# Kernel tuning notes

Hardware: AMD Instinct MI355X
Metric: run time of the kernel (lower is better)

## Reference

```python
import jax, jax.numpy as jnp
import numpy as np

N, E = 100000, 1600000
F_IN, F_HID, F_OUT = 512, 128, 16


def gcn_conv(x, W, b, src, dst, ew):
    """PyG GCNConv: h = x @ W; add self loops (weight 1); symmetric norm
    D^-1/2 A D^-1/2; aggregate messages to dst; add bias."""
    n = x.shape[0]
    loop = jnp.arange(n, dtype=src.dtype)
    s = jnp.concatenate([src, loop])
    d = jnp.concatenate([dst, loop])
    w = jnp.concatenate([ew, jnp.ones((n,), ew.dtype)])
    deg = jax.ops.segment_sum(w, d, num_segments=n)           # [N]
    dinv = jnp.where(deg > 0, jax.lax.rsqrt(deg), 0.0)
    norm = dinv[s] * w * dinv[d]                              # [E+N]
    h = x @ W                                                 # [N, out]
    out = jax.ops.segment_sum(h[s] * norm[:, None], d, num_segments=n)
    return out + b


def setup_inputs() -> dict:
    key = jax.random.key(0)
    k = jax.random.split(key, 5)
    x = jax.random.normal(k[0], (N, F_IN), jnp.float32)
    edge_index = jax.random.randint(k[1], (2, E), 0, N, jnp.int32)
    edge_weight = jnp.ones((E,), jnp.float32)
    W1 = jax.random.normal(k[2], (F_IN, F_HID), jnp.float32) * (1.0 / np.sqrt(F_IN))
    b1 = jnp.zeros((F_HID,), jnp.float32)
    W2 = jax.random.normal(k[3], (F_HID, F_OUT), jnp.float32) * (1.0 / np.sqrt(F_HID))
    b2 = jnp.zeros((F_OUT,), jnp.float32)
    return {"x": x, "edge_index": edge_index, "edge_weight": edge_weight,
            "W1": W1, "b1": b1, "W2": W2, "b2": b2}


def reference(x, edge_index, edge_weight, W1, b1, W2, b2):
    # eval mode: dropout is identity; use_ln=False, layer_norm_first=False
    src, dst = edge_index[0], edge_index[1]
    h = jax.nn.relu(gcn_conv(x, W1, b1, src, dst, edge_weight))
    logits = gcn_conv(h, W2, b2, src, dst, edge_weight)
    return jax.nn.log_softmax(logits, axis=1)
```

## Files before the change

kernel.cpp:

```cpp
#include <hip/hip_runtime.h>
#include <math.h>


#define F_IN 512
#define F_HID 128
#define F_OUT 16

__global__ __launch_bounds__(256) void k_cnt_deg(const int* __restrict__ dst,
                                                 const float* __restrict__ ew,
                                                 int* __restrict__ cnt,
                                                 float* __restrict__ degw, int E) {
  int e = blockIdx.x * 256 + threadIdx.x;
  if (e < E) {
    int d = dst[e];
    atomicAdd(&cnt[d], 1);
    atomicAdd(&degw[d], ew[e]);
  }
}

__global__ __launch_bounds__(256) void k_dinv(float* __restrict__ deg, int n) {
  int i = blockIdx.x * 256 + threadIdx.x;
  if (i < n) {
    float d = deg[i] + 1.0f;
    deg[i] = d > 0.f ? rsqrtf(d) : 0.f;
  }
}

__global__ __launch_bounds__(256) void k_scan1(const int* __restrict__ cnt,
                                               int* __restrict__ rowptr,
                                               int* __restrict__ bsum, int n) {
  __shared__ int sd[256];
  const int t = threadIdx.x;
  const int i = blockIdx.x * 256 + t;
  int v = (i < n) ? cnt[i] : 0;
  sd[t] = v;
  __syncthreads();
#pragma unroll
  for (int off = 1; off < 256; off <<= 1) {
    int add = (t >= off) ? sd[t - off] : 0;
    __syncthreads();
    sd[t] += add;
    __syncthreads();
  }
  if (i < n) rowptr[i] = sd[t] - v;
  if (t == 255) bsum[blockIdx.x] = sd[255];
}

__global__ __launch_bounds__(512) void k_scan2(int* __restrict__ bsum, int nb) {
  __shared__ int sd[512];
  const int t = threadIdx.x;
  int v = (t < nb) ? bsum[t] : 0;
  sd[t] = v;
  __syncthreads();
#pragma unroll
  for (int off = 1; off < 512; off <<= 1) {
    int add = (t >= off) ? sd[t - off] : 0;
    __syncthreads();
    sd[t] += add;
    __syncthreads();
  }
  if (t < nb) bsum[t] = sd[t] - v;
}

__global__ __launch_bounds__(256) void k_scan3(int* __restrict__ rowptr,
                                               const int* __restrict__ bsum,
                                               int* __restrict__ cursor,
                                               int n, int E) {
  int i = blockIdx.x * 256 + threadIdx.x;
  if (i < n) {
    int r = rowptr[i] + bsum[blockIdx.x];
    rowptr[i] = r;
    cursor[i] = r;
  }
  if (i == 0) rowptr[n] = E;
}

__global__ __launch_bounds__(256) void k_scatter(const int* __restrict__ src,
                                                 const int* __restrict__ dst,
                                                 const float* __restrict__ ew,
                                                 const float* __restrict__ dinv,
                                                 int* __restrict__ cursor,
                                                 int* __restrict__ es,
                                                 float* __restrict__ en, int E) {
  int e = blockIdx.x * 256 + threadIdx.x;
  if (e >= E) return;
  int s = src[e], d = dst[e];
  int pos = atomicAdd(&cursor[d], 1);
  es[pos] = s;
  en[pos] = dinv[s] * ew[e] * dinv[d];
}

__global__ __launch_bounds__(256) void k_gemm1(const float* __restrict__ A,
                                               const float* __restrict__ B,
                                               float* __restrict__ C, int n) {
  __shared__ float As[16][68];
  __shared__ float Bs[16][128];
  const int tid = threadIdx.x;
  const int bm = blockIdx.x * 64;
  const int ty = tid >> 4;
  const int tx = tid & 15;
  const int am = tid >> 2, ak = (tid & 3) << 2;
  const int bk = tid >> 4, bx = tid & 15;
  float acc[4][8];
#pragma unroll
  for (int i = 0; i < 4; ++i)
#pragma unroll
    for (int j = 0; j < 8; ++j) acc[i][j] = 0.f;

  for (int k0 = 0; k0 < F_IN; k0 += 16) {
    float4 av = make_float4(0.f, 0.f, 0.f, 0.f);
    if (bm + am < n)
      av = *reinterpret_cast<const float4*>(&A[(size_t)(bm + am) * F_IN + k0 + ak]);
    float4 b0 = *reinterpret_cast<const float4*>(&B[(size_t)(k0 + bk) * F_HID + bx * 4]);
    float4 b1 = *reinterpret_cast<const float4*>(&B[(size_t)(k0 + bk) * F_HID + 64 + bx * 4]);
    __syncthreads();
    As[ak + 0][am] = av.x;
    As[ak + 1][am] = av.y;
    As[ak + 2][am] = av.z;
    As[ak + 3][am] = av.w;
    *reinterpret_cast<float4*>(&Bs[bk][bx * 4]) = b0;
    *reinterpret_cast<float4*>(&Bs[bk][64 + bx * 4]) = b1;
    __syncthreads();
#pragma unroll
    for (int kk = 0; kk < 16; ++kk) {
      float4 a4 = *reinterpret_cast<const float4*>(&As[kk][ty * 4]);
      float4 p0 = *reinterpret_cast<const float4*>(&Bs[kk][tx * 4]);
      float4 p1 = *reinterpret_cast<const float4*>(&Bs[kk][64 + tx * 4]);
      float a[4] = {a4.x, a4.y, a4.z, a4.w};
      float b[8] = {p0.x, p0.y, p0.z, p0.w, p1.x, p1.y, p1.z, p1.w};
#pragma unroll
      for (int i = 0; i < 4; ++i)
#pragma unroll
        for (int j = 0; j < 8; ++j) acc[i][j] = fmaf(a[i], b[j], acc[i][j]);
    }
  }
#pragma unroll
  for (int i = 0; i < 4; ++i) {
    int r = bm + ty * 4 + i;
    if (r < n) {
      *reinterpret_cast<float4*>(&C[(size_t)r * F_HID + tx * 4]) =
          make_float4(acc[i][0], acc[i][1], acc[i][2], acc[i][3]);
      *reinterpret_cast<float4*>(&C[(size_t)r * F_HID + 64 + tx * 4]) =
          make_float4(acc[i][4], acc[i][5], acc[i][6], acc[i][7]);
    }
  }
}

__global__ __launch_bounds__(256) void k_pull128(const int* __restrict__ rowptr,
                                                 const int* __restrict__ es,
                                                 const float* __restrict__ en,
                                                 const float* __restrict__ h1,
                                                 const float* __restrict__ dinv,
                                                 const float* __restrict__ b1,
                                                 float* __restrict__ out, int n) {
  int node = blockIdx.x * 4 + (threadIdx.x >> 6);
  if (node >= n) return;
  int lane = threadIdx.x & 63;
  int beg = rowptr[node], end = rowptr[node + 1];
  float ax = 0.f, ay = 0.f;
  int j = beg;
  for (; j + 1 < end; j += 2) {
    int s0 = es[j], s1 = es[j + 1];
    float n0 = en[j], n1 = en[j + 1];
    float2 v0 = *reinterpret_cast<const float2*>(&h1[(size_t)s0 * F_HID + lane * 2]);
    float2 v1 = *reinterpret_cast<const float2*>(&h1[(size_t)s1 * F_HID + lane * 2]);
    ax = fmaf(v0.x, n0, ax);
    ay = fmaf(v0.y, n0, ay);
    ax = fmaf(v1.x, n1, ax);
    ay = fmaf(v1.y, n1, ay);
  }
  if (j < end) {
    int s0 = es[j];
    float n0 = en[j];
    float2 v0 = *reinterpret_cast<const float2*>(&h1[(size_t)s0 * F_HID + lane * 2]);
    ax = fmaf(v0.x, n0, ax);
    ay = fmaf(v0.y, n0, ay);
  }
  float di = dinv[node], sl = di * di;
  float2 hv = *reinterpret_cast<const float2*>(&h1[(size_t)node * F_HID + lane * 2]);
  float2 bv = *reinterpret_cast<const float2*>(&b1[lane * 2]);
  float2 r;
  r.x = fmaxf(fmaf(hv.x, sl, ax) + bv.x, 0.f);
  r.y = fmaxf(fmaf(hv.y, sl, ay) + bv.y, 0.f);
  *reinterpret_cast<float2*>(&out[(size_t)node * F_HID + lane * 2]) = r;
}

__global__ __launch_bounds__(256) void k_gemm2(const float* __restrict__ h,
                                               const float* __restrict__ W2,
                                               float* __restrict__ out, int n) {
  __shared__ float w2s[F_HID * F_OUT];
  for (int t = threadIdx.x; t < F_HID * F_OUT; t += 256) w2s[t] = W2[t];
  __syncthreads();
  int t = blockIdx.x * 256 + threadIdx.x;
  int i = t >> 4, j = t & 15;
  if (i >= n) return;
  const float4* row = reinterpret_cast<const float4*>(&h[(size_t)i * F_HID]);
  float acc = 0.f;
#pragma unroll
  for (int k4 = 0; k4 < F_HID / 4; ++k4) {
    float4 r = row[k4];
    acc = fmaf(r.x, w2s[(k4 * 4 + 0) * F_OUT + j], acc);
    acc = fmaf(r.y, w2s[(k4 * 4 + 1) * F_OUT + j], acc);
    acc = fmaf(r.z, w2s[(k4 * 4 + 2) * F_OUT + j], acc);
    acc = fmaf(r.w, w2s[(k4 * 4 + 3) * F_OUT + j], acc);
  }
  out[t] = acc;
}

__global__ __launch_bounds__(256) void k_pull16_out(const int* __restrict__ rowptr,
                                                    const int* __restrict__ es,
                                                    const float* __restrict__ en,
                                                    const float* __restrict__ h2,
                                                    const float* __restrict__ dinv,
                                                    const float* __restrict__ b2,
                                                    float* __restrict__ out, int n) {
  int node = blockIdx.x * 16 + (threadIdx.x >> 4);
  if (node >= n) return;
  int lane = threadIdx.x & 15;
  int beg = rowptr[node], end = rowptr[node + 1];
  float acc = 0.f;
  int j = beg;
  for (; j + 1 < end; j += 2) {
    float v0 = h2[(size_t)es[j] * F_OUT + lane];
    float v1 = h2[(size_t)es[j + 1] * F_OUT + lane];
    acc = fmaf(v0, en[j], acc);
    acc = fmaf(v1, en[j + 1], acc);
  }
  if (j < end) acc = fmaf(h2[(size_t)es[j] * F_OUT + lane], en[j], acc);
  float di = dinv[node];
  float v = fmaf(h2[(size_t)node * F_OUT + lane], di * di, acc) + b2[lane];
  float m = v;
#pragma unroll
  for (int off = 8; off; off >>= 1) m = fmaxf(m, __shfl_xor(m, off, 16));
  float ex = expf(v - m);
  float s = ex;
#pragma unroll
  for (int off = 8; off; off >>= 1) s += __shfl_xor(s, off, 16);
  out[(size_t)node * F_OUT + lane] = v - m - logf(s);
}

extern "C" void kernel_launch(void* const* d_in, const int* in_sizes, int n_in,
                              void* d_out, int out_size, void* d_ws, size_t ws_size,
                              hipStream_t stream) {
  const float* x  = (const float*)d_in[0];
  const int*   ei = (const int*)d_in[1];
  const float* ew = (const float*)d_in[2];
  const float* W1 = (const float*)d_in[3];
  const float* b1 = (const float*)d_in[4];
  const float* W2 = (const float*)d_in[5];
  const float* b2 = (const float*)d_in[6];
  float* out = (float*)d_out;

  const int fhid = in_sizes[4];
  const int fin  = in_sizes[3] / fhid;
  const int n = in_sizes[0] / fin;
  const int E = in_sizes[2];
  const int* src = ei;
  const int* dst = ei + E;

  const size_t nr = (size_t)((n + 255) & ~255);
  float* ws     = (float*)d_ws;
  float* dinv   = ws;
  float* h1     = dinv + nr;
  float* agg1   = h1 + (size_t)n * F_HID;
  float* h2     = agg1 + (size_t)n * F_HID;
  int*   cnt    = (int*)(h2 + (size_t)n * F_OUT);
  int*   rowptr = cnt + nr;
  int*   bsum   = rowptr + nr;
  int*   es     = bsum + 512;
  float* en     = (float*)(es + E);

  hipMemsetAsync(dinv, 0, nr * 4, stream);
  hipMemsetAsync(cnt, 0, nr * 4, stream);

  const int gE = (E + 255) / 256;
  const int gN = (n + 255) / 256;
  k_cnt_deg<<<gE, 256, 0, stream>>>(dst, ew, cnt, dinv, E);
  k_dinv<<<gN, 256, 0, stream>>>(dinv, n);
  k_scan1<<<gN, 256, 0, stream>>>(cnt, rowptr, bsum, n);
  k_scan2<<<1, 512, 0, stream>>>(bsum, gN);
  k_scan3<<<gN, 256, 0, stream>>>(rowptr, bsum, cnt, n, E);
  k_scatter<<<gE, 256, 0, stream>>>(src, dst, ew, dinv, cnt, es, en, E);
  k_gemm1<<<(n + 63) / 64, 256, 0, stream>>>(x, W1, h1, n);
  k_pull128<<<(n + 3) / 4, 256, 0, stream>>>(rowptr, es, en, h1, dinv, b1, agg1, n);
  k_gemm2<<<(n * F_OUT + 255) / 256, 256, 0, stream>>>(agg1, W2, h2, n);
  k_pull16_out<<<(n + 15) / 16, 256, 0, stream>>>(rowptr, es, en, h2, dinv, b2, out, n);
}
```

Baseline: 865.3 us.

## Run first-layer GEMM on bf16 MFMA with double-buffered LDS staging

Measured after the change: 811.8 us. 1.07x faster.

```diff
diff --git a/kernel.cpp b/kernel.cpp
--- a/kernel.cpp
+++ b/kernel.cpp
@@ -5,6 +5,16 @@
 #define F_IN 512
 #define F_HID 128
 #define F_OUT 16
+
+typedef __attribute__((ext_vector_type(8))) short bf16x8;
+typedef __attribute__((ext_vector_type(4))) float f32x4;
+
+__device__ __forceinline__ unsigned short f2bf(float f) {
+  union { float f; unsigned u; } c;
+  c.f = f;
+  unsigned u = c.u;
+  return (unsigned short)((u + 0x7FFFu + ((u >> 16) & 1u)) >> 16);
+}
 
 __global__ __launch_bounds__(256) void k_cnt_deg(const int* __restrict__ dst,
                                                  const float* __restrict__ ew,
@@ -90,60 +100,96 @@
   en[pos] = dinv[s] * ew[e] * dinv[d];
 }
 
-__global__ __launch_bounds__(256) void k_gemm1(const float* __restrict__ A,
-                                               const float* __restrict__ B,
-                                               float* __restrict__ C, int n) {
-  __shared__ float As[16][68];
-  __shared__ float Bs[16][128];
+__global__ __launch_bounds__(256) void k_w1t(const float* __restrict__ W1,
+                                             unsigned short* __restrict__ W1T) {
+  int t = blockIdx.x * 256 + threadIdx.x;
+  int k = t >> 7, c = t & 127;
+  W1T[(size_t)c * F_IN + k] = f2bf(W1[t]);
+}
+
+__global__ __launch_bounds__(256) void k_gemm1m(const float* __restrict__ A,
+                                                const unsigned short* __restrict__ BT,
+                                                float* __restrict__ C, int n) {
+  __shared__ unsigned short As[2][128][72];
   const int tid = threadIdx.x;
-  const int bm = blockIdx.x * 64;
-  const int ty = tid >> 4;
-  const int tx = tid & 15;
-  const int am = tid >> 2, ak = (tid & 3) << 2;
-  const int bk = tid >> 4, bx = tid & 15;
-  float acc[4][8];
-#pragma unroll
-  for (int i = 0; i < 4; ++i)
-#pragma unroll
-    for (int j = 0; j < 8; ++j) acc[i][j] = 0.f;
-
-  for (int k0 = 0; k0 < F_IN; k0 += 16) {
-    float4 av = make_float4(0.f, 0.f, 0.f, 0.f);
-    if (bm + am < n)
-      av = *reinterpret_cast<const float4*>(&A[(size_t)(bm + am) * F_IN + k0 + ak]);
-    float4 b0 = *reinterpret_cast<const float4*>(&B[(size_t)(k0 + bk) * F_HID + bx * 4]);
-    float4 b1 = *reinterpret_cast<const float4*>(&B[(size_t)(k0 + bk) * F_HID + 64 + bx * 4]);
-    __syncthreads();
-    As[ak + 0][am] = av.x;
-    As[ak + 1][am] = av.y;
-    As[ak + 2][am] = av.z;
-    As[ak + 3][am] = av.w;
-    *reinterpret_cast<float4*>(&Bs[bk][bx * 4]) = b0;
-    *reinterpret_cast<float4*>(&Bs[bk][64 + bx * 4]) = b1;
-    __syncthreads();
-#pragma unroll
-    for (int kk = 0; kk < 16; ++kk) {
-      float4 a4 = *reinterpret_cast<const float4*>(&As[kk][ty * 4]);
-      float4 p0 = *reinterpret_cast<const float4*>(&Bs[kk][tx * 4]);
-      float4 p1 = *reinterpret_cast<const float4*>(&Bs[kk][64 + tx * 4]);
-      float a[4] = {a4.x, a4.y, a4.z, a4.w};
-      float b[8] = {p0.x, p0.y, p0.z, p0.w, p1.x, p1.y, p1.z, p1.w};
-#pragma unroll
-      for (int i = 0; i < 4; ++i)
-#pragma unroll
-        for (int j = 0; j < 8; ++j) acc[i][j] = fmaf(a[i], b[j], acc[i][j]);
+  const int wave = tid >> 6, lane = tid & 63;
+  const int lg = lane >> 4, lr = lane & 15;
+  const int bm = blockIdx.x * 128;
+  const int srow = tid >> 1;
+  const int scol = (tid & 1) * 32;
+  const bool sok = (bm + srow) < n;
+  const float* abase = &A[(size_t)(bm + srow) * F_IN + scol];
+
+  f32x4 acc[2][8];
+#pragma unroll
+  for (int i = 0; i < 2; ++i)
+#pragma unroll
+    for (int j = 0; j < 8; ++j) acc[i][j] = (f32x4){0.f, 0.f, 0.f, 0.f};
+
+  float4 stg[8];
+#define ISSUE(K0)                                                            \
+  {                                                                          \
+    _Pragma("unroll") for (int i = 0; i < 8; ++i)                            \
+        stg[i] = sok ? *reinterpret_cast<const float4*>(abase + (K0) + i * 4)\
+                     : make_float4(0.f, 0.f, 0.f, 0.f);                      \
+  }
+#define WRITE_LDS(BUF)                                                       \
+  {                                                                          \
+    _Pragma("unroll") for (int i = 0; i < 4; ++i) {                          \
+      bf16x8 w;                                                              \
+      w[0] = (short)f2bf(stg[2 * i].x);                                      \
+      w[1] = (short)f2bf(stg[2 * i].y);                                      \
+      w[2] = (short)f2bf(stg[2 * i].z);                                      \
+      w[3] = (short)f2bf(stg[2 * i].w);                                      \
+      w[4] = (short)f2bf(stg[2 * i + 1].x);                                  \
+      w[5] = (short)f2bf(stg[2 * i + 1].y);                                  \
+      w[6] = (short)f2bf(stg[2 * i + 1].z);                                  \
+      w[7] = (short)f2bf(stg[2 * i + 1].w);                                  \
+      *reinterpret_cast<bf16x8*>(&As[BUF][srow][scol + i * 8]) = w;          \
+    }                                                                        \
+  }
+
+  ISSUE(0)
+  WRITE_LDS(0)
+  __syncthreads();
+
+  for (int t = 0; t < 8; ++t) {
+    const int buf = t & 1;
+    if (t < 7) ISSUE((t + 1) * 64)
+    const int k0 = t * 64;
+#pragma unroll
+    for (int s = 0; s < 2; ++s) {
+      bf16x8 a0 = *reinterpret_cast<bf16x8*>(&As[buf][wave * 32 + lr][s * 32 + lg * 8]);
+      bf16x8 a1 = *reinterpret_cast<bf16x8*>(&As[buf][wave * 32 + 16 + lr][s * 32 + lg * 8]);
+      bf16x8 b[8];
+#pragma unroll
+      for (int nf = 0; nf < 8; ++nf)
+        b[nf] = *reinterpret_cast<const bf16x8*>(
+            &BT[(size_t)(nf * 16 + lr) * F_IN + k0 + s * 32 + lg * 8]);
+#pragma unroll
+      for (int nf = 0; nf < 8; ++nf) {
+        acc[0][nf] = __builtin_amdgcn_mfma_f32_16x16x32_bf16(a0, b[nf], acc[0][nf], 0, 0, 0);
+        acc[1][nf] = __builtin_amdgcn_mfma_f32_16x16x32_bf16(a1, b[nf], acc[1][nf], 0, 0, 0);
+      }
     }
-  }
-#pragma unroll
-  for (int i = 0; i < 4; ++i) {
-    int r = bm + ty * 4 + i;
-    if (r < n) {
-      *reinterpret_cast<float4*>(&C[(size_t)r * F_HID + tx * 4]) =
-          make_float4(acc[i][0], acc[i][1], acc[i][2], acc[i][3]);
-      *reinterpret_cast<float4*>(&C[(size_t)r * F_HID + 64 + tx * 4]) =
-          make_float4(acc[i][4], acc[i][5], acc[i][6], acc[i][7]);
+    if (t < 7) WRITE_LDS(buf ^ 1)
+    __syncthreads();
+  }
+
+  const int rbase = bm + wave * 32 + lg * 4;
+#pragma unroll
+  for (int mf = 0; mf < 2; ++mf)
+#pragma unroll
+    for (int r = 0; r < 4; ++r) {
+      int row = rbase + mf * 16 + r;
+      if (row < n) {
+#pragma unroll
+        for (int nf = 0; nf < 8; ++nf)
+          C[(size_t)row * F_HID + nf * 16 + lr] = acc[mf][nf][r];
+      }
     }
-  }
+#undef ISSUE
+#undef WRITE_LDS
 }
 
 __global__ __launch_bounds__(256) void k_pull128(const int* __restrict__ rowptr,
@@ -269,19 +315,21 @@
   int*   bsum   = rowptr + nr;
   int*   es     = bsum + 512;
   float* en     = (float*)(es + E);
+  unsigned short* W1T = (unsigned short*)(en + E);
 
   hipMemsetAsync(dinv, 0, nr * 4, stream);
   hipMemsetAsync(cnt, 0, nr * 4, stream);
 
   const int gE = (E + 255) / 256;
   const int gN = (n + 255) / 256;
+  k_w1t<<<(F_IN * F_HID) / 256, 256, 0, stream>>>(W1, W1T);
   k_cnt_deg<<<gE, 256, 0, stream>>>(dst, ew, cnt, dinv, E);
   k_dinv<<<gN, 256, 0, stream>>>(dinv, n);
   k_scan1<<<gN, 256, 0, stream>>>(cnt, rowptr, bsum, n);
   k_scan2<<<1, 512, 0, stream>>>(bsum, gN);
   k_scan3<<<gN, 256, 0, stream>>>(rowptr, bsum, cnt, n, E);
   k_scatter<<<gE, 256, 0, stream>>>(src, dst, ew, dinv, cnt, es, en, E);
-  k_gemm1<<<(n + 63) / 64, 256, 0, stream>>>(x, W1, h1, n);
+  k_gemm1m<<<(n + 127) / 128, 256, 0, stream>>>(x, W1T, h1, n);
   k_pull128<<<(n + 3) / 4, 256, 0, stream>>>(rowptr, es, en, h1, dinv, b1, agg1, n);
   k_gemm2<<<(n * F_OUT + 255) / 256, 256, 0, stream>>>(agg1, W2, h2, n);
   k_pull16_out<<<(n + 15) / 16, 256, 0, stream>>>(rowptr, es, en, h2, dinv, b2, out, n);
```
